# Performance work log

Hardware: AMD Instinct MI355X
Metric: run time of the kernel (lower is better)

## Reference

```python
import jax, jax.numpy as jnp
import numpy as np

FLOW_NUM = 2048
H = 64  # lstm_output_dim
NOISE_DIM = 3


def _w(key, shape, s=0.08):
    return (jax.random.normal(key, shape, dtype=jnp.float32) * s)


def setup_inputs() -> dict:
    key = jax.random.key(0)
    ks = jax.random.split(key, 20)
    d = {
        "noise": jax.random.normal(ks[0], (FLOW_NUM, NOISE_DIM), dtype=jnp.float32),
        "w_ih0": _w(ks[1], (4 * H, NOISE_DIM)),
        "w_hh0": _w(ks[2], (4 * H, H)),
        "b_ih0": _w(ks[3], (4 * H,)),
        "b_hh0": _w(ks[4], (4 * H,)),
        "w_ih1": _w(ks[5], (4 * H, H)),
        "w_hh1": _w(ks[6], (4 * H, H)),
        "b_ih1": _w(ks[7], (4 * H,)),
        "b_hh1": _w(ks[8], (4 * H,)),
        "w_ih2": _w(ks[9], (4 * H, H)),
        "w_hh2": _w(ks[10], (4 * H, H)),
        "b_ih2": _w(ks[11], (4 * H,)),
        "b_hh2": _w(ks[12], (4 * H,)),
        "fc1_w": _w(ks[13], (32, H)),
        "fc1_b": _w(ks[14], (32,)),
        "fc2_w": _w(ks[15], (16, 32)),
        "fc2_b": _w(ks[16], (16,)),
        "fc3_w": _w(ks[17], (3, 16)),
        "fc3_b": _w(ks[18], (3,)),
        "flow_length": 500,
    }
    return d


def _lstm_cell(x, h, c, w_ih, w_hh, b_ih, b_hh):
    # PyTorch gate order: input, forget, cell(g), output
    gates = x @ w_ih.T + h @ w_hh.T + (b_ih + b_hh)
    i, f, g, o = jnp.split(gates, 4, axis=-1)
    c_new = jax.nn.sigmoid(f) * c + jax.nn.sigmoid(i) * jnp.tanh(g)
    h_new = jax.nn.sigmoid(o) * jnp.tanh(c_new)
    return h_new, c_new


def reference(noise, w_ih0, w_hh0, b_ih0, b_hh0,
              w_ih1, w_hh1, b_ih1, b_hh1,
              w_ih2, w_hh2, b_ih2, b_hh2,
              fc1_w, fc1_b, fc2_w, fc2_b, fc3_w, fc3_b,
              flow_length):
    layers = [(w_ih0, w_hh0, b_ih0, b_hh0),
              (w_ih1, w_hh1, b_ih1, b_hh1),
              (w_ih2, w_hh2, b_ih2, b_hh2)]
    n = noise.shape[0]
    h0 = jnp.zeros((3, n, H), dtype=noise.dtype)
    c0 = jnp.zeros((3, n, H), dtype=noise.dtype)

    def step(carry, _):
        x, h, c = carry
        inp = x
        hs, cs = [], []
        for l, (wi, wh, bi, bh) in enumerate(layers):
            h_l, c_l = _lstm_cell(inp, h[l], c[l], wi, wh, bi, bh)
            hs.append(h_l)
            cs.append(c_l)
            inp = h_l
        # MLP head (Dropout is identity in eval mode); LeakyReLU slope 0.01
        y = jax.nn.leaky_relu(inp @ fc1_w.T + fc1_b)
        y = jax.nn.leaky_relu(y @ fc2_w.T + fc2_b)
        y = jax.nn.leaky_relu(y @ fc3_w.T + fc3_b)
        return (y, jnp.stack(hs), jnp.stack(cs)), y

    _, flow = jax.lax.scan(step, (noise, h0, c0), None, length=flow_length)
    # flow: [flow_length, flow_num, 3] -> [flow_num, flow_length, 3]
    return jnp.swapaxes(flow, 0, 1)
```

## Files before the change

### kernel.cpp

```cpp
#include <hip/hip_runtime.h>

#define NT 512

typedef _Float16 f16x8 __attribute__((ext_vector_type(8)));
typedef _Float16 f16x4 __attribute__((ext_vector_type(4)));
typedef float    f32x4 __attribute__((ext_vector_type(4)));

#define MFMA(a, b, c) __builtin_amdgcn_mfma_f32_16x16x32_f16((a), (b), (c), 0, 0, 0)

#if __has_builtin(__builtin_amdgcn_exp2f)
__device__ __forceinline__ float fexp(float x) { return __builtin_amdgcn_exp2f(x * 1.4426950408889634f); }
#else
__device__ __forceinline__ float fexp(float x) { return __expf(x); }
#endif
#if __has_builtin(__builtin_amdgcn_rcpf)
__device__ __forceinline__ float frcp(float x) { return __builtin_amdgcn_rcpf(x); }
#else
__device__ __forceinline__ float frcp(float x) { return 1.0f / x; }
#endif
__device__ __forceinline__ float sigm(float x)  { return frcp(1.0f + fexp(-x)); }
__device__ __forceinline__ float tanh_(float x) { return 1.0f - 2.0f * frcp(1.0f + fexp(2.0f * x)); }
__device__ __forceinline__ float lrelu(float x) { return x > 0.0f ? x : 0.01f * x; }

__device__ __forceinline__ f16x8 ld8(const float* p) {
    const float4* q = (const float4*)p;
    float4 a = q[0], b = q[1];
    f16x8 r = { (_Float16)a.x, (_Float16)a.y, (_Float16)a.z, (_Float16)a.w,
                (_Float16)b.x, (_Float16)b.y, (_Float16)b.z, (_Float16)b.w };
    return r;
}

__global__ __launch_bounds__(NT, 2)
void gen_kernel(
    const float* __restrict__ noise,
    const float* __restrict__ w_ih0, const float* __restrict__ w_hh0,
    const float* __restrict__ b_ih0, const float* __restrict__ b_hh0,
    const float* __restrict__ w_ih1, const float* __restrict__ w_hh1,
    const float* __restrict__ b_ih1, const float* __restrict__ b_hh1,
    const float* __restrict__ w_ih2, const float* __restrict__ w_hh2,
    const float* __restrict__ b_ih2, const float* __restrict__ b_hh2,
    const float* __restrict__ fc1_w, const float* __restrict__ fc1_b,
    const float* __restrict__ fc2_w, const float* __restrict__ fc2_b,
    const float* __restrict__ fc3_w, const float* __restrict__ fc3_b,
    const int*   __restrict__ flow_len_p,
    float* __restrict__ out)
{
    __shared__ _Float16 sh[3][2][16][72] __attribute__((aligned(16)));
    __shared__ _Float16 sx [16][40] __attribute__((aligned(16)));
    __shared__ _Float16 sy1[16][40] __attribute__((aligned(16)));
    __shared__ _Float16 sy2[16][40] __attribute__((aligned(16)));

    const int tid  = threadIdx.x;
    const int l    = tid & 63;
    const int w    = tid >> 6;
    const int ls   = l & 15;
    const int lj   = l >> 4;
    const int base = blockIdx.x * 8;
    const int T    = flow_len_p[0];

    const int gA   = ls & 3;
    const int rA0  = gA * 64 + 4 * (2 * w + 0) + (ls >> 2);
    const int rA1  = gA * 64 + 4 * (2 * w + 1) + (ls >> 2);

    f16x8 A1[2][4], A2[2][4], A0[2][3];
#pragma unroll
    for (int kc = 0; kc < 2; ++kc) {
        A1[0][kc]     = ld8(w_ih1 + rA0 * 64 + 32 * kc + 8 * lj);
        A1[1][kc]     = ld8(w_ih1 + rA1 * 64 + 32 * kc + 8 * lj);
        A1[0][2 + kc] = ld8(w_hh1 + rA0 * 64 + 32 * kc + 8 * lj);
        A1[1][2 + kc] = ld8(w_hh1 + rA1 * 64 + 32 * kc + 8 * lj);
        A2[0][kc]     = ld8(w_ih2 + rA0 * 64 + 32 * kc + 8 * lj);
        A2[1][kc]     = ld8(w_ih2 + rA1 * 64 + 32 * kc + 8 * lj);
        A2[0][2 + kc] = ld8(w_hh2 + rA0 * 64 + 32 * kc + 8 * lj);
        A2[1][2 + kc] = ld8(w_hh2 + rA1 * 64 + 32 * kc + 8 * lj);
        A0[0][kc]     = ld8(w_hh0 + rA0 * 64 + 32 * kc + 8 * lj);
        A0[1][kc]     = ld8(w_hh0 + rA1 * 64 + 32 * kc + 8 * lj);
    }
#pragma unroll
    for (int tt = 0; tt < 2; ++tt) {
        const int r = tt ? rA1 : rA0;
        f16x8 v;
#pragma unroll
        for (int i = 0; i < 8; ++i) {
            int kl = 8 * lj + i;
            float x = (kl < 3) ? w_ih0[r * 3 + kl]
                    : (kl == 3) ? (b_ih0[r] + b_hh0[r]) : 0.0f;
            v[i] = (_Float16)x;
        }
        A0[tt][2] = v;
    }
    f16x8 F1[2][2], F2, F3;
#pragma unroll
    for (int tt = 0; tt < 2; ++tt)
#pragma unroll
        for (int kc = 0; kc < 2; ++kc)
            F1[tt][kc] = ld8(fc1_w + (16 * tt + ls) * 64 + 32 * kc + 8 * lj);
    F2 = ld8(fc2_w + ls * 32 + 8 * lj);
    {
        f16x8 v;
#pragma unroll
        for (int i = 0; i < 8; ++i) {
            int k = 8 * lj + i;
            v[i] = (_Float16)((ls < 3 && k < 16) ? fc3_w[ls * 16 + k] : 0.0f);
        }
        F3 = v;
    }
    const int uc0 = 8 * w + lj, uc1 = 8 * w + 4 + lj;
    float b1v[2][4], b2v[2][4];
#pragma unroll
    for (int g = 0; g < 4; ++g) {
        b1v[0][g] = b_ih1[g * 64 + uc0] + b_hh1[g * 64 + uc0];
        b1v[1][g] = b_ih1[g * 64 + uc1] + b_hh1[g * 64 + uc1];
        b2v[0][g] = b_ih2[g * 64 + uc0] + b_hh2[g * 64 + uc0];
        b2v[1][g] = b_ih2[g * 64 + uc1] + b_hh2[g * 64 + uc1];
    }
    float hb1a[4], hb1b[4], hb2[4];
#pragma unroll
    for (int r = 0; r < 4; ++r) {
        hb1a[r] = fc1_b[4 * lj + r];
        hb1b[r] = fc1_b[16 + 4 * lj + r];
        hb2[r]  = fc2_b[4 * lj + r];
    }
    float fb3[3] = { fc3_b[0], fc3_b[1], fc3_b[2] };

    for (int i = tid; i < 3 * 2 * 16 * 72; i += NT) ((_Float16*)sh)[i]  = (_Float16)0.0f;
    for (int i = tid; i < 16 * 40; i += NT) {
        ((_Float16*)sx)[i]  = (_Float16)0.0f;
        ((_Float16*)sy1)[i] = (_Float16)0.0f;
        ((_Float16*)sy2)[i] = (_Float16)0.0f;
    }
    __syncthreads();
    if (tid < 16) sx[tid][3] = (_Float16)1.0f;
    if (tid < 24) {
        int s = tid / 3, d = tid % 3;
        sx[s][d] = (_Float16)noise[(base + s) * 3 + d];
    }

    float c0[2] = {0, 0}, c1[2] = {0, 0}, c2[2] = {0, 0};
    __syncthreads();

#define RD(L, p, kb) (*(const f16x8*)&sh[L][p][ls][(kb) + 8 * lj])

#define ACT(acc, bv, cref, L, p, u) {                                          \
        float gi = acc[0] + bv[0], gf = acc[1] + bv[1];                        \
        float gg = acc[2] + bv[2], go = acc[3] + bv[3];                        \
        cref = sigm(gf) * cref + sigm(gi) * tanh_(gg);                         \
        sh[L][p][ls][u] = (_Float16)(sigm(go) * tanh_(cref)); }

    {
        f16x8 bx = *(const f16x8*)&sx[ls][8 * lj];
        f32x4 a0 = {0, 0, 0, 0}, a1 = {0, 0, 0, 0};
        a0 = MFMA(A0[0][2], bx, a0);
        a1 = MFMA(A0[1][2], bx, a1);
        float zb[4] = {0, 0, 0, 0};
        ACT(a0, zb, c0[0], 0, 0, uc0)
        ACT(a1, zb, c0[1], 0, 0, uc1)
    }
    __syncthreads();

    for (int t = 0; t < T; ++t) {
        const int pc = t & 1, pp = pc ^ 1;
        {
            f16x8 q0 = RD(0, pc, 0), q1 = RD(0, pc, 32);
            f16x8 q2 = RD(1, pp, 0), q3 = RD(1, pp, 32);
            f32x4 a0 = {0, 0, 0, 0}, a1 = {0, 0, 0, 0};
            a0 = MFMA(A1[0][0], q0, a0); a1 = MFMA(A1[1][0], q0, a1);
            a0 = MFMA(A1[0][1], q1, a0); a1 = MFMA(A1[1][1], q1, a1);
            a0 = MFMA(A1[0][2], q2, a0); a1 = MFMA(A1[1][2], q2, a1);
            a0 = MFMA(A1[0][3], q3, a0); a1 = MFMA(A1[1][3], q3, a1);
            ACT(a0, b1v[0], c1[0], 1, pc, uc0)
            ACT(a1, b1v[1], c1[1], 1, pc, uc1)
        }
        __syncthreads();
        {
            f16x8 q0 = RD(1, pc, 0), q1 = RD(1, pc, 32);
            f16x8 q2 = RD(2, pp, 0), q3 = RD(2, pp, 32);
            f32x4 a0 = {0, 0, 0, 0}, a1 = {0, 0, 0, 0};
            a0 = MFMA(A2[0][0], q0, a0); a1 = MFMA(A2[1][0], q0, a1);
            a0 = MFMA(A2[0][1], q1, a0); a1 = MFMA(A2[1][1], q1, a1);
            a0 = MFMA(A2[0][2], q2, a0); a1 = MFMA(A2[1][2], q2, a1);
            a0 = MFMA(A2[0][3], q3, a0); a1 = MFMA(A2[1][3], q3, a1);
            ACT(a0, b2v[0], c2[0], 2, pc, uc0)
            ACT(a1, b2v[1], c2[1], 2, pc, uc1)
        }
        __syncthreads();
        f32x4 h0a = {0, 0, 0, 0}, h0b = {0, 0, 0, 0};
        {
            f16x8 q0 = RD(0, pc, 0), q1 = RD(0, pc, 32);
            h0a = MFMA(A0[0][0], q0, h0a); h0b = MFMA(A0[1][0], q0, h0b);
            h0a = MFMA(A0[0][1], q1, h0a); h0b = MFMA(A0[1][1], q1, h0b);
        }
        if (w == 0) {
            f16x8 bh0 = RD(2, pc, 0), bh1 = RD(2, pc, 32);
            f32x4 y1a = {0, 0, 0, 0}, y1b = {0, 0, 0, 0};
            y1a = MFMA(F1[0][0], bh0, y1a); y1b = MFMA(F1[1][0], bh0, y1b);
            y1a = MFMA(F1[0][1], bh1, y1a); y1b = MFMA(F1[1][1], bh1, y1b);
            f16x4 v;
#pragma unroll
            for (int r = 0; r < 4; ++r) v[r] = (_Float16)lrelu(y1a[r] + hb1a[r]);
            *(f16x4*)&sy1[ls][4 * lj] = v;
#pragma unroll
            for (int r = 0; r < 4; ++r) v[r] = (_Float16)lrelu(y1b[r] + hb1b[r]);
            *(f16x4*)&sy1[ls][16 + 4 * lj] = v;
            f16x8 by1 = *(const f16x8*)&sy1[ls][8 * lj];
            f32x4 y2 = {0, 0, 0, 0};
            y2 = MFMA(F2, by1, y2);
#pragma unroll
            for (int r = 0; r < 4; ++r) v[r] = (_Float16)lrelu(y2[r] + hb2[r]);
            *(f16x4*)&sy2[ls][4 * lj] = v;
            f16x8 by2 = *(const f16x8*)&sy2[ls][8 * lj];
            f32x4 y3 = {0, 0, 0, 0};
            y3 = MFMA(F3, by2, y3);
            if (lj == 0) {
                float o0 = lrelu(y3[0] + fb3[0]);
                float o1 = lrelu(y3[1] + fb3[1]);
                float o2 = lrelu(y3[2] + fb3[2]);
                sx[ls][0] = (_Float16)o0;
                sx[ls][1] = (_Float16)o1;
                sx[ls][2] = (_Float16)o2;
                if (ls < 8) {
                    float* op = out + ((size_t)(base + ls) * T + t) * 3;
                    op[0] = o0; op[1] = o1; op[2] = o2;
                }
            }
        }
        __syncthreads();
        {
            f16x8 bx = *(const f16x8*)&sx[ls][8 * lj];
            h0a = MFMA(A0[0][2], bx, h0a);
            h0b = MFMA(A0[1][2], bx, h0b);
            float zb[4] = {0, 0, 0, 0};
            ACT(h0a, zb, c0[0], 0, pp, uc0)
            ACT(h0b, zb, c0[1], 0, pp, uc1)
        }
        __syncthreads();
    }
}

extern "C" void kernel_launch(void* const* d_in, const int* in_sizes, int n_in,
                              void* d_out, int out_size, void* d_ws, size_t ws_size,
                              hipStream_t stream) {
    const float* noise = (const float*)d_in[0];
    const float* w_ih0 = (const float*)d_in[1];
    const float* w_hh0 = (const float*)d_in[2];
    const float* b_ih0 = (const float*)d_in[3];
    const float* b_hh0 = (const float*)d_in[4];
    const float* w_ih1 = (const float*)d_in[5];
    const float* w_hh1 = (const float*)d_in[6];
    const float* b_ih1 = (const float*)d_in[7];
    const float* b_hh1 = (const float*)d_in[8];
    const float* w_ih2 = (const float*)d_in[9];
    const float* w_hh2 = (const float*)d_in[10];
    const float* b_ih2 = (const float*)d_in[11];
    const float* b_hh2 = (const float*)d_in[12];
    const float* fc1w  = (const float*)d_in[13];
    const float* fc1b  = (const float*)d_in[14];
    const float* fc2w  = (const float*)d_in[15];
    const float* fc2b  = (const float*)d_in[16];
    const float* fc3w  = (const float*)d_in[17];
    const float* fc3b  = (const float*)d_in[18];
    const int*   flp   = (const int*)d_in[19];

    gen_kernel<<<dim3(256), dim3(NT), 0, stream>>>(
        noise, w_ih0, w_hh0, b_ih0, b_hh0,
        w_ih1, w_hh1, b_ih1, b_hh1,
        w_ih2, w_hh2, b_ih2, b_hh2,
        fc1w, fc1b, fc2w, fc2b, fc3w, fc3b,
        flp, (float*)d_out);
}
```

Measured before the change: 975.4 us.

## Halve block size, compute MLP head redundantly per wave via shuffles, drop a barrier

Each block now handles 4 flows with 4 waves, and each wave owns 16 hidden units instead of 8. The grid doubles to 512 blocks. The MLP head now runs in every wave, with the intermediate activations passed between lanes by shuffles instead of through shared memory. The new head output feeds the layer-0 input directly in registers, so one __syncthreads per timestep disappears. In exchange, each wave does redundant head work, register pressure roughly doubles from holding 4 tiles of weights, and half of each MFMA's N=16 columns are padding for 4 flows.

```diff
diff --git a/kernel.cpp b/kernel.cpp
--- a/kernel.cpp
+++ b/kernel.cpp
@@ -1,9 +1,8 @@
 #include <hip/hip_runtime.h>
 
-#define NT 512
+#define NT 256
 
 typedef _Float16 f16x8 __attribute__((ext_vector_type(8)));
-typedef _Float16 f16x4 __attribute__((ext_vector_type(4)));
 typedef float    f32x4 __attribute__((ext_vector_type(4)));
 
 #define MFMA(a, b, c) __builtin_amdgcn_mfma_f32_16x16x32_f16((a), (b), (c), 0, 0, 0)
@@ -28,6 +27,13 @@
     f16x8 r = { (_Float16)a.x, (_Float16)a.y, (_Float16)a.z, (_Float16)a.w,
                 (_Float16)b.x, (_Float16)b.y, (_Float16)b.z, (_Float16)b.w };
     return r;
+}
+__device__ __forceinline__ unsigned pack2(float a, float b) {
+    union { _Float16 h[2]; unsigned u; } x;
+    x.h[0] = (_Float16)a; x.h[1] = (_Float16)b; return x.u;
+}
+__device__ __forceinline__ _Float16 half_of(unsigned v, int sel) {
+    union { unsigned u; _Float16 h[2]; } x; x.u = v; return x.h[sel];
 }
 
 __global__ __launch_bounds__(NT, 2)
@@ -46,48 +52,47 @@
     float* __restrict__ out)
 {
     __shared__ _Float16 sh[3][2][16][72] __attribute__((aligned(16)));
-    __shared__ _Float16 sx [16][40] __attribute__((aligned(16)));
-    __shared__ _Float16 sy1[16][40] __attribute__((aligned(16)));
-    __shared__ _Float16 sy2[16][40] __attribute__((aligned(16)));
 
     const int tid  = threadIdx.x;
     const int l    = tid & 63;
     const int w    = tid >> 6;
     const int ls   = l & 15;
     const int lj   = l >> 4;
-    const int base = blockIdx.x * 8;
+    const int base = blockIdx.x * 4;
     const int T    = flow_len_p[0];
 
-    const int gA   = ls & 3;
-    const int rA0  = gA * 64 + 4 * (2 * w + 0) + (ls >> 2);
-    const int rA1  = gA * 64 + 4 * (2 * w + 1) + (ls >> 2);
-
-    f16x8 A1[2][4], A2[2][4], A0[2][3];
-#pragma unroll
-    for (int kc = 0; kc < 2; ++kc) {
-        A1[0][kc]     = ld8(w_ih1 + rA0 * 64 + 32 * kc + 8 * lj);
-        A1[1][kc]     = ld8(w_ih1 + rA1 * 64 + 32 * kc + 8 * lj);
-        A1[0][2 + kc] = ld8(w_hh1 + rA0 * 64 + 32 * kc + 8 * lj);
-        A1[1][2 + kc] = ld8(w_hh1 + rA1 * 64 + 32 * kc + 8 * lj);
-        A2[0][kc]     = ld8(w_ih2 + rA0 * 64 + 32 * kc + 8 * lj);
-        A2[1][kc]     = ld8(w_ih2 + rA1 * 64 + 32 * kc + 8 * lj);
-        A2[0][2 + kc] = ld8(w_hh2 + rA0 * 64 + 32 * kc + 8 * lj);
-        A2[1][2 + kc] = ld8(w_hh2 + rA1 * 64 + 32 * kc + 8 * lj);
-        A0[0][kc]     = ld8(w_hh0 + rA0 * 64 + 32 * kc + 8 * lj);
-        A0[1][kc]     = ld8(w_hh0 + rA1 * 64 + 32 * kc + 8 * lj);
-    }
-#pragma unroll
-    for (int tt = 0; tt < 2; ++tt) {
-        const int r = tt ? rA1 : rA0;
-        f16x8 v;
-#pragma unroll
-        for (int i = 0; i < 8; ++i) {
-            int kl = 8 * lj + i;
-            float x = (kl < 3) ? w_ih0[r * 3 + kl]
-                    : (kl == 3) ? (b_ih0[r] + b_hh0[r]) : 0.0f;
-            v[i] = (_Float16)x;
-        }
-        A0[tt][2] = v;
+    f16x8 A1[4][4], A2[4][4], A0[4][3];
+    float b1v[4][4], b2v[4][4];
+    int   uc[4];
+#pragma unroll
+    for (int tt = 0; tt < 4; ++tt) {
+        const int r = (ls & 3) * 64 + 4 * (4 * w + tt) + (ls >> 2);
+#pragma unroll
+        for (int kc = 0; kc < 2; ++kc) {
+            A1[tt][kc]     = ld8(w_ih1 + r * 64 + 32 * kc + 8 * lj);
+            A1[tt][2 + kc] = ld8(w_hh1 + r * 64 + 32 * kc + 8 * lj);
+            A2[tt][kc]     = ld8(w_ih2 + r * 64 + 32 * kc + 8 * lj);
+            A2[tt][2 + kc] = ld8(w_hh2 + r * 64 + 32 * kc + 8 * lj);
+            A0[tt][kc]     = ld8(w_hh0 + r * 64 + 32 * kc + 8 * lj);
+        }
+        {
+            f16x8 v;
+#pragma unroll
+            for (int i = 0; i < 8; ++i) {
+                int kl = 8 * lj + i;
+                float x = (kl < 3) ? w_ih0[r * 3 + kl]
+                        : (kl == 3) ? (b_ih0[r] + b_hh0[r]) : 0.0f;
+                v[i] = (_Float16)x;
+            }
+            A0[tt][2] = v;
+        }
+        const int u = 16 * w + 4 * tt + lj;
+        uc[tt] = u;
+#pragma unroll
+        for (int g = 0; g < 4; ++g) {
+            b1v[tt][g] = b_ih1[g * 64 + u] + b_hh1[g * 64 + u];
+            b2v[tt][g] = b_ih2[g * 64 + u] + b_hh2[g * 64 + u];
+        }
     }
     f16x8 F1[2][2], F2, F3;
 #pragma unroll
@@ -105,56 +110,47 @@
         }
         F3 = v;
     }
-    const int uc0 = 8 * w + lj, uc1 = 8 * w + 4 + lj;
-    float b1v[2][4], b2v[2][4];
-#pragma unroll
-    for (int g = 0; g < 4; ++g) {
-        b1v[0][g] = b_ih1[g * 64 + uc0] + b_hh1[g * 64 + uc0];
-        b1v[1][g] = b_ih1[g * 64 + uc1] + b_hh1[g * 64 + uc1];
-        b2v[0][g] = b_ih2[g * 64 + uc0] + b_hh2[g * 64 + uc0];
-        b2v[1][g] = b_ih2[g * 64 + uc1] + b_hh2[g * 64 + uc1];
-    }
-    float hb1a[4], hb1b[4], hb2[4];
+    float hb1a[4], hb1b[4], hb2r[4];
 #pragma unroll
     for (int r = 0; r < 4; ++r) {
         hb1a[r] = fc1_b[4 * lj + r];
         hb1b[r] = fc1_b[16 + 4 * lj + r];
-        hb2[r]  = fc2_b[4 * lj + r];
-    }
-    float fb3[3] = { fc3_b[0], fc3_b[1], fc3_b[2] };
-
-    for (int i = tid; i < 3 * 2 * 16 * 72; i += NT) ((_Float16*)sh)[i]  = (_Float16)0.0f;
-    for (int i = tid; i < 16 * 40; i += NT) {
-        ((_Float16*)sx)[i]  = (_Float16)0.0f;
-        ((_Float16*)sy1)[i] = (_Float16)0.0f;
-        ((_Float16*)sy2)[i] = (_Float16)0.0f;
-    }
+        hb2r[r] = fc2_b[4 * lj + r];
+    }
+    const float fb3_0 = fc3_b[0], fb3_1 = fc3_b[1], fb3_2 = fc3_b[2];
+
+    for (int i = tid; i < 3 * 2 * 16 * 72; i += NT) ((_Float16*)sh)[i] = (_Float16)0.0f;
     __syncthreads();
-    if (tid < 16) sx[tid][3] = (_Float16)1.0f;
-    if (tid < 24) {
-        int s = tid / 3, d = tid % 3;
-        sx[s][d] = (_Float16)noise[(base + s) * 3 + d];
-    }
-
-    float c0[2] = {0, 0}, c1[2] = {0, 0}, c2[2] = {0, 0};
-    __syncthreads();
+
+    float c0[4] = {0,0,0,0}, c1[4] = {0,0,0,0}, c2[4] = {0,0,0,0};
+    const float zb[4] = {0, 0, 0, 0};
 
 #define RD(L, p, kb) (*(const f16x8*)&sh[L][p][ls][(kb) + 8 * lj])
 
-#define ACT(acc, bv, cref, L, p, u) {                                          \
-        float gi = acc[0] + bv[0], gf = acc[1] + bv[1];                        \
-        float gg = acc[2] + bv[2], go = acc[3] + bv[3];                        \
+#define ACT(a, bv, cref, L, p, u) {                                            \
+        float gi = a[0] + bv[0], gf = a[1] + bv[1];                            \
+        float gg = a[2] + bv[2], go = a[3] + bv[3];                            \
         cref = sigm(gf) * cref + sigm(gi) * tanh_(gg);                         \
         sh[L][p][ls][u] = (_Float16)(sigm(go) * tanh_(cref)); }
 
     {
-        f16x8 bx = *(const f16x8*)&sx[ls][8 * lj];
-        f32x4 a0 = {0, 0, 0, 0}, a1 = {0, 0, 0, 0};
-        a0 = MFMA(A0[0][2], bx, a0);
-        a1 = MFMA(A0[1][2], bx, a1);
-        float zb[4] = {0, 0, 0, 0};
-        ACT(a0, zb, c0[0], 0, 0, uc0)
-        ACT(a1, zb, c0[1], 0, 0, uc1)
+        f16x8 bx;
+#pragma unroll
+        for (int i = 0; i < 8; ++i) bx[i] = (_Float16)0.0f;
+        if (lj == 0) {
+            if (ls < 4) {
+                bx[0] = (_Float16)noise[(base + ls) * 3 + 0];
+                bx[1] = (_Float16)noise[(base + ls) * 3 + 1];
+                bx[2] = (_Float16)noise[(base + ls) * 3 + 2];
+            }
+            bx[3] = (_Float16)1.0f;
+        }
+#pragma unroll
+        for (int tt = 0; tt < 4; ++tt) {
+            f32x4 a = {0, 0, 0, 0};
+            a = MFMA(A0[tt][2], bx, a);
+            ACT(a, zb, c0[tt], 0, 0, uc[tt])
+        }
     }
     __syncthreads();
 
@@ -163,75 +159,91 @@
         {
             f16x8 q0 = RD(0, pc, 0), q1 = RD(0, pc, 32);
             f16x8 q2 = RD(1, pp, 0), q3 = RD(1, pp, 32);
-            f32x4 a0 = {0, 0, 0, 0}, a1 = {0, 0, 0, 0};
-            a0 = MFMA(A1[0][0], q0, a0); a1 = MFMA(A1[1][0], q0, a1);
-            a0 = MFMA(A1[0][1], q1, a0); a1 = MFMA(A1[1][1], q1, a1);
-            a0 = MFMA(A1[0][2], q2, a0); a1 = MFMA(A1[1][2], q2, a1);
-            a0 = MFMA(A1[0][3], q3, a0); a1 = MFMA(A1[1][3], q3, a1);
-            ACT(a0, b1v[0], c1[0], 1, pc, uc0)
-            ACT(a1, b1v[1], c1[1], 1, pc, uc1)
+#pragma unroll
+            for (int tt = 0; tt < 4; ++tt) {
+                f32x4 a = {0, 0, 0, 0};
+                a = MFMA(A1[tt][0], q0, a); a = MFMA(A1[tt][1], q1, a);
+                a = MFMA(A1[tt][2], q2, a); a = MFMA(A1[tt][3], q3, a);
+                ACT(a, b1v[tt], c1[tt], 1, pc, uc[tt])
+            }
         }
         __syncthreads();
         {
             f16x8 q0 = RD(1, pc, 0), q1 = RD(1, pc, 32);
             f16x8 q2 = RD(2, pp, 0), q3 = RD(2, pp, 32);
-            f32x4 a0 = {0, 0, 0, 0}, a1 = {0, 0, 0, 0};
-            a0 = MFMA(A2[0][0], q0, a0); a1 = MFMA(A2[1][0], q0, a1);
-            a0 = MFMA(A2[0][1], q1, a0); a1 = MFMA(A2[1][1], q1, a1);
-            a0 = MFMA(A2[0][2], q2, a0); a1 = MFMA(A2[1][2], q2, a1);
-            a0 = MFMA(A2[0][3], q3, a0); a1 = MFMA(A2[1][3], q3, a1);
-            ACT(a0, b2v[0], c2[0], 2, pc, uc0)
-            ACT(a1, b2v[1], c2[1], 2, pc, uc1)
+#pragma unroll
+            for (int tt = 0; tt < 4; ++tt) {
+                f32x4 a = {0, 0, 0, 0};
+                a = MFMA(A2[tt][0], q0, a); a = MFMA(A2[tt][1], q1, a);
+                a = MFMA(A2[tt][2], q2, a); a = MFMA(A2[tt][3], q3, a);
+                ACT(a, b2v[tt], c2[tt], 2, pc, uc[tt])
+            }
         }
         __syncthreads();
-        f32x4 h0a = {0, 0, 0, 0}, h0b = {0, 0, 0, 0};
-        {
-            f16x8 q0 = RD(0, pc, 0), q1 = RD(0, pc, 32);
-            h0a = MFMA(A0[0][0], q0, h0a); h0b = MFMA(A0[1][0], q0, h0b);
-            h0a = MFMA(A0[0][1], q1, h0a); h0b = MFMA(A0[1][1], q1, h0b);
-        }
-        if (w == 0) {
-            f16x8 bh0 = RD(2, pc, 0), bh1 = RD(2, pc, 32);
+        {
+            f16x8 e0 = RD(2, pc, 0), e1 = RD(2, pc, 32);
             f32x4 y1a = {0, 0, 0, 0}, y1b = {0, 0, 0, 0};
-            y1a = MFMA(F1[0][0], bh0, y1a); y1b = MFMA(F1[1][0], bh0, y1b);
-            y1a = MFMA(F1[0][1], bh1, y1a); y1b = MFMA(F1[1][1], bh1, y1b);
-            f16x4 v;
-#pragma unroll
-            for (int r = 0; r < 4; ++r) v[r] = (_Float16)lrelu(y1a[r] + hb1a[r]);
-            *(f16x4*)&sy1[ls][4 * lj] = v;
-#pragma unroll
-            for (int r = 0; r < 4; ++r) v[r] = (_Float16)lrelu(y1b[r] + hb1b[r]);
-            *(f16x4*)&sy1[ls][16 + 4 * lj] = v;
-            f16x8 by1 = *(const f16x8*)&sy1[ls][8 * lj];
+            y1a = MFMA(F1[0][0], e0, y1a); y1a = MFMA(F1[0][1], e1, y1a);
+            y1b = MFMA(F1[1][0], e0, y1b); y1b = MFMA(F1[1][1], e1, y1b);
+            unsigned pk[4];
+#pragma unroll
+            for (int r = 0; r < 4; ++r)
+                pk[r] = pack2(lrelu(y1a[r] + hb1a[r]), lrelu(y1b[r] + hb1b[r]));
+            const int laneA = ls + 32 * (lj & 1);
+            const int sel   = lj >> 1;
+            f16x8 by1;
+#pragma unroll
+            for (int i = 0; i < 4; ++i) {
+                unsigned v = (unsigned)__shfl((int)pk[i], laneA);
+                by1[i] = half_of(v, sel);
+            }
+#pragma unroll
+            for (int i = 0; i < 4; ++i) {
+                unsigned v = (unsigned)__shfl((int)pk[i], laneA + 16);
+                by1[4 + i] = half_of(v, sel);
+            }
             f32x4 y2 = {0, 0, 0, 0};
             y2 = MFMA(F2, by1, y2);
-#pragma unroll
-            for (int r = 0; r < 4; ++r) v[r] = (_Float16)lrelu(y2[r] + hb2[r]);
-            *(f16x4*)&sy2[ls][4 * lj] = v;
-            f16x8 by2 = *(const f16x8*)&sy2[ls][8 * lj];
+            float y2r[4];
+#pragma unroll
+            for (int r = 0; r < 4; ++r) y2r[r] = lrelu(y2[r] + hb2r[r]);
+            f16x8 by2;
+#pragma unroll
+            for (int i = 0; i < 4; ++i) {
+                float v = __shfl(y2r[i], laneA);
+                by2[i] = (lj < 2) ? (_Float16)v : (_Float16)0.0f;
+            }
+#pragma unroll
+            for (int i = 0; i < 4; ++i) {
+                float v = __shfl(y2r[i], laneA + 16);
+                by2[4 + i] = (lj < 2) ? (_Float16)v : (_Float16)0.0f;
+            }
             f32x4 y3 = {0, 0, 0, 0};
             y3 = MFMA(F3, by2, y3);
+            f16x8 bx;
+#pragma unroll
+            for (int i = 0; i < 8; ++i) bx[i] = (_Float16)0.0f;
+            float o0 = 0.0f, o1 = 0.0f, o2 = 0.0f;
             if (lj == 0) {
-                float o0 = lrelu(y3[0] + fb3[0]);
-                float o1 = lrelu(y3[1] + fb3[1]);
-                float o2 = lrelu(y3[2] + fb3[2]);
-                sx[ls][0] = (_Float16)o0;
-                sx[ls][1] = (_Float16)o1;
-                sx[ls][2] = (_Float16)o2;
-                if (ls < 8) {
-                    float* op = out + ((size_t)(base + ls) * T + t) * 3;
-                    op[0] = o0; op[1] = o1; op[2] = o2;
-                }
-            }
-        }
-        __syncthreads();
-        {
-            f16x8 bx = *(const f16x8*)&sx[ls][8 * lj];
-            h0a = MFMA(A0[0][2], bx, h0a);
-            h0b = MFMA(A0[1][2], bx, h0b);
-            float zb[4] = {0, 0, 0, 0};
-            ACT(h0a, zb, c0[0], 0, pp, uc0)
-            ACT(h0b, zb, c0[1], 0, pp, uc1)
+                o0 = lrelu(y3[0] + fb3_0);
+                o1 = lrelu(y3[1] + fb3_1);
+                o2 = lrelu(y3[2] + fb3_2);
+                bx[0] = (_Float16)o0; bx[1] = (_Float16)o1;
+                bx[2] = (_Float16)o2; bx[3] = (_Float16)1.0f;
+            }
+            if (w == 0 && lj == 0 && ls < 4) {
+                float* op = out + ((size_t)(base + ls) * T + t) * 3;
+                op[0] = o0; op[1] = o1; op[2] = o2;
+            }
+            f16x8 g0 = RD(0, pc, 0), g1 = RD(0, pc, 32);
+#pragma unroll
+            for (int tt = 0; tt < 4; ++tt) {
+                f32x4 a = {0, 0, 0, 0};
+                a = MFMA(A0[tt][0], g0, a);
+                a = MFMA(A0[tt][1], g1, a);
+                a = MFMA(A0[tt][2], bx, a);
+                ACT(a, zb, c0[tt], 0, pp, uc[tt])
+            }
         }
         __syncthreads();
     }
@@ -261,7 +273,7 @@
     const float* fc3b  = (const float*)d_in[18];
     const int*   flp   = (const int*)d_in[19];
 
-    gen_kernel<<<dim3(256), dim3(NT), 0, stream>>>(
+    gen_kernel<<<dim3(512), dim3(NT), 0, stream>>>(
         noise, w_ih0, w_hh0, b_ih0, b_hh0,
         w_ih1, w_hh1, b_ih1, b_hh1,
         w_ih2, w_hh2, b_ih2, b_hh2,
```

After: 2.579 ms. 2.64x slower.
